# Optimization experiments

Hardware: AMD Instinct MI355X
Metric: run time of the kernel (lower is better)

The kernel has to match this reference:

```python
import jax, jax.numpy as jnp
import numpy as np

V_SRC = 32000; V_TGT = 32000; E = 512; H = 1024; N = 32; LS = 64; LT = 48; PAD = 0


def setup_inputs() -> dict:
    key = jax.random.key(0)
    ks = jax.random.split(key, 12)
    def rn(k, shape, scale):
        return jax.random.normal(k, shape, dtype=jnp.float32) * jnp.float32(scale)
    return {
        "src": jax.random.randint(ks[0], (N, LS), 0, V_SRC, dtype=jnp.int32),
        "tgt": jax.random.randint(ks[1], (N, LT), 0, V_TGT, dtype=jnp.int32),
        "enc_embed": rn(ks[2], (V_SRC, E), 0.02),
        "enc_Wi": rn(ks[3], (E, 4 * H), 1.0 / np.sqrt(E)),
        "enc_Wh": rn(ks[4], (H, 4 * H), 1.0 / np.sqrt(H)),
        "enc_b": jnp.zeros((4 * H,), jnp.float32),
        "dec_embed": rn(ks[5], (V_TGT, E), 0.02),
        "dec_Wi": rn(ks[6], (E + H, 4 * H), 1.0 / np.sqrt(E + H)),
        "dec_Wh": rn(ks[7], (H, 4 * H), 1.0 / np.sqrt(H)),
        "dec_b": jnp.zeros((4 * H,), jnp.float32),
        "attn_W": rn(ks[8], (H, H), 1.0 / np.sqrt(H)),
        "attn_b": jnp.zeros((H,), jnp.float32),
        "h2o_W": rn(ks[9], (H, V_TGT), 1.0 / np.sqrt(H)),
        "h2o_b": jnp.zeros((V_TGT,), jnp.float32),
    }


def _lstm_step(h, c, x, Wi, Wh, b):
    # fused gate GEMM; gate order i, f, g, o (matches the 8 separate Linears)
    gates = x @ Wi + h @ Wh + b
    i, f, g, o = jnp.split(gates, 4, axis=-1)
    c_new = jax.nn.sigmoid(f) * c + jax.nn.sigmoid(i) * jnp.tanh(g)
    h_new = jax.nn.sigmoid(o) * jnp.tanh(c_new)
    return h_new, c_new


def reference(src, tgt, enc_embed, enc_Wi, enc_Wh, enc_b,
              dec_embed, dec_Wi, dec_Wh, dec_b,
              attn_W, attn_b, h2o_W, h2o_b):
    n = src.shape[0]
    h0 = jnp.zeros((n, H), enc_Wi.dtype)
    c0 = jnp.zeros((n, H), enc_Wi.dtype)

    # ---- encoder: scan over source timesteps ----
    emb_src = enc_embed[src]                       # [N,LS,E]
    def estep(carry, x_t):
        h, c = carry
        h, c = _lstm_step(h, c, x_t, enc_Wi, enc_Wh, enc_b)
        return (h, c), h
    (h, c), enc_h = jax.lax.scan(estep, (h0, c0), jnp.swapaxes(emb_src, 0, 1))
    enc_h = jnp.swapaxes(enc_h, 0, 1)              # [N,LS,H]
    mask = (src == PAD)                            # True = PAD

    # Attention linear on encoder_outputs is step-invariant -> precompute once
    energy = enc_h @ attn_W + attn_b               # [N,LS,H]

    # ---- decoder: teacher forcing (ratio=1.0) over tgt[:, :-1] ----
    def dstep(carry, tok):
        h, c = carry
        emb = dec_embed[tok]                       # [N,E]
        scores = jnp.einsum('nlh,nh->nl', energy, h)
        scores = jnp.where(mask, jnp.float32(-1e9), scores)
        w = jax.nn.softmax(scores, axis=1)         # [N,LS]
        ctx = jnp.einsum('nl,nlh->nh', w, enc_h)   # [N,H]
        h, c = _lstm_step(h, c, jnp.concatenate([emb, ctx], axis=-1),
                          dec_Wi, dec_Wh, dec_b)
        out = jax.nn.log_softmax(h @ h2o_W + h2o_b, axis=-1)
        return (h, c), out
    _, outs = jax.lax.scan(dstep, (h, c), jnp.swapaxes(tgt[:, :-1], 0, 1))
    return jnp.swapaxes(outs, 0, 1)                # [N, LT-1, V_TGT]
```

## Files before the change

### kernel.cpp

```cpp
#include <hip/hip_runtime.h>


using u16 = unsigned short;
using u32 = unsigned int;
using bf16x8 = __attribute__((ext_vector_type(8))) __bf16;
using f32x4  = __attribute__((ext_vector_type(4))) float;
using u32x4  = __attribute__((ext_vector_type(4))) unsigned int;
using u32x2  = __attribute__((ext_vector_type(2))) unsigned int;

__device__ __forceinline__ u16 f2bf(float x) {
  u32 u = __float_as_uint(x);
  u32 r = (u + 0x7FFFu + ((u >> 16) & 1u)) >> 16;
  return (u16)r;
}
__device__ __forceinline__ float bf2f(u16 b) { return __uint_as_float(((u32)b) << 16); }
__device__ __forceinline__ float sigm(float x) { return 1.f / (1.f + expf(-x)); }

__device__ __forceinline__ f32x4 mfma16(u32x4 a, u32x4 b, f32x4 c) {
  return __builtin_amdgcn_mfma_f32_16x16x32_bf16(
      __builtin_bit_cast(bf16x8, a), __builtin_bit_cast(bf16x8, b), c, 0, 0, 0);
}

__global__ __launch_bounds__(256)
void k_transpose_split(const float* __restrict__ W, int K, int N,
                       u16* __restrict__ Thi, u16* __restrict__ Tlo,
                       int ldT, int koff)
{
  __shared__ float tile[32][33];
  const int k0 = blockIdx.y << 5, n0 = blockIdx.x << 5;
  const int tx = threadIdx.x & 31, ty = threadIdx.x >> 5;
  #pragma unroll
  for (int i = ty; i < 32; i += 8)
    tile[i][tx] = W[(size_t)(k0 + i) * N + n0 + tx];
  __syncthreads();
  #pragma unroll
  for (int i = ty; i < 32; i += 8) {
    float v = tile[tx][i];
    u16 hi = f2bf(v);
    size_t di = (size_t)(n0 + i) * ldT + koff + k0 + tx;
    Thi[di] = hi;
    if (Tlo) Tlo[di] = f2bf(v - bf2f(hi));
  }
}

__global__ __launch_bounds__(256)
void k_embed(const float* __restrict__ emb, const int* __restrict__ toks,
             int tokStride, int nRows, u16* __restrict__ A)
{
  int id = blockIdx.x * 256 + threadIdx.x;
  if (id >= nRows * 64) return;
  int r = id >> 6, c8 = (id & 63) << 3;
  int t = r >> 5, n = r & 31;
  int tok = toks[n * tokStride + t];
  const float* s = emb + (size_t)tok * 512 + c8;
  f32x4 x0 = *(const f32x4*)s;
  f32x4 x1 = *(const f32x4*)(s + 4);
  u32x4 w;
  w[0] = (u32)f2bf(x0[0]) | ((u32)f2bf(x0[1]) << 16);
  w[1] = (u32)f2bf(x0[2]) | ((u32)f2bf(x0[3]) << 16);
  w[2] = (u32)f2bf(x1[0]) | ((u32)f2bf(x1[1]) << 16);
  w[3] = (u32)f2bf(x1[2]) | ((u32)f2bf(x1[3]) << 16);
  *(u32x4*)(A + (size_t)r * 512 + c8) = w;
}

template<bool X2, int OUTMAP>
__global__ __launch_bounds__(256)
void gemm_k(const u16* __restrict__ Ah, const u16* __restrict__ Al,
            const u16* __restrict__ Bh, const u16* __restrict__ Bl,
            const float* __restrict__ bias, float* __restrict__ C,
            int M, int N, int K, int Mstore)
{
  const int lane = threadIdx.x & 63, wave = threadIdx.x >> 6;
  const int m0 = blockIdx.y * 128 + (wave >> 1) * 64;
  const int n0 = blockIdx.x * 128 + (wave & 1) * 64;
  const int fr = lane & 15, fq = lane >> 4;
  const f32x4 z = {0.f, 0.f, 0.f, 0.f};
  f32x4 acc[4][4];
  #pragma unroll
  for (int i = 0; i < 4; i++)
    #pragma unroll
    for (int j = 0; j < 4; j++) acc[i][j] = z;

  const size_t a_base = (size_t)(m0 + fr) * K + fq * 8;
  const size_t b_base = (size_t)(n0 + fr) * K + fq * 8;
  for (int k0 = 0; k0 < K; k0 += 32) {
    u32x4 a[4], b[4], a2[4], b2[4];
    #pragma unroll
    for (int i = 0; i < 4; i++) a[i] = *(const u32x4*)(Ah + a_base + (size_t)i * 16 * K + k0);
    #pragma unroll
    for (int j = 0; j < 4; j++) b[j] = *(const u32x4*)(Bh + b_base + (size_t)j * 16 * K + k0);
    if constexpr (X2) {
      #pragma unroll
      for (int i = 0; i < 4; i++) a2[i] = *(const u32x4*)(Al + a_base + (size_t)i * 16 * K + k0);
      #pragma unroll
      for (int j = 0; j < 4; j++) b2[j] = *(const u32x4*)(Bl + b_base + (size_t)j * 16 * K + k0);
    }
    #pragma unroll
    for (int i = 0; i < 4; i++)
      #pragma unroll
      for (int j = 0; j < 4; j++) {
        acc[i][j] = mfma16(a[i], b[j], acc[i][j]);
        if constexpr (X2) {
          acc[i][j] = mfma16(a[i], b2[j], acc[i][j]);
          acc[i][j] = mfma16(a2[i], b[j], acc[i][j]);
        }
      }
  }
  #pragma unroll
  for (int i = 0; i < 4; i++) {
    int row_b = m0 + i * 16 + fq * 4;
    #pragma unroll
    for (int j = 0; j < 4; j++) {
      int col = n0 + j * 16 + fr;
      float bv = bias ? bias[col] : 0.f;
      #pragma unroll
      for (int r = 0; r < 4; r++) {
        int row = row_b + r;
        if (row < Mstore) {
          float v = acc[i][j][r] + bv;
          if (OUTMAP) {
            int nn = row & 31, tt = row >> 5;
            C[(size_t)(nn * 47 + tt) * N + col] = v;
          } else {
            C[(size_t)row * N + col] = v;
          }
        }
      }
    }
  }
}

__global__ __launch_bounds__(256)
void rec_gemm(const u16* __restrict__ Ah, const u16* __restrict__ Al,
              const u16* __restrict__ Bh, const u16* __restrict__ Bl,
              float* __restrict__ partial, int KK, int kchunk)
{
  const int lane = threadIdx.x & 63, wave = threadIdx.x >> 6;
  const int n0 = blockIdx.x * 256 + wave * 64;
  const int fr = lane & 15, fq = lane >> 4;
  const int ks = blockIdx.y * kchunk, ke = ks + kchunk;
  const f32x4 z = {0.f, 0.f, 0.f, 0.f};
  f32x4 acc[2][4];
  #pragma unroll
  for (int i = 0; i < 2; i++)
    #pragma unroll
    for (int j = 0; j < 4; j++) acc[i][j] = z;

  for (int k0 = ks; k0 < ke; k0 += 32) {
    u32x4 a[2], a2[2], b[4], b2[4];
    #pragma unroll
    for (int i = 0; i < 2; i++) {
      size_t o = (size_t)(i * 16 + fr) * KK + k0 + fq * 8;
      a[i]  = *(const u32x4*)(Ah + o);
      a2[i] = *(const u32x4*)(Al + o);
    }
    #pragma unroll
    for (int j = 0; j < 4; j++) {
      size_t o = (size_t)(n0 + j * 16 + fr) * KK + k0 + fq * 8;
      b[j]  = *(const u32x4*)(Bh + o);
      b2[j] = *(const u32x4*)(Bl + o);
    }
    #pragma unroll
    for (int i = 0; i < 2; i++)
      #pragma unroll
      for (int j = 0; j < 4; j++) {
        acc[i][j] = mfma16(a[i], b[j], acc[i][j]);
        acc[i][j] = mfma16(a[i], b2[j], acc[i][j]);
        acc[i][j] = mfma16(a2[i], b[j], acc[i][j]);
      }
  }
  float* pb = partial + (size_t)blockIdx.y * 32 * 4096;
  #pragma unroll
  for (int i = 0; i < 2; i++)
    #pragma unroll
    for (int j = 0; j < 4; j++)
      #pragma unroll
      for (int r = 0; r < 4; r++) {
        int row = i * 16 + fq * 4 + r;
        int col = n0 + j * 16 + fr;
        pb[(size_t)row * 4096 + col] = acc[i][j][r];
      }
}

__global__ __launch_bounds__(256)
void point_enc(const float* __restrict__ partial, const float* __restrict__ Xi,
               float* __restrict__ c, float* __restrict__ hf,
               u16* __restrict__ hhi, u16* __restrict__ hlo, int usep)
{
  int idx = blockIdx.x * 256 + threadIdx.x;
  int n = idx >> 10, hh = idx & 1023;
  size_t xb = (size_t)n * 4096 + hh;
  float g[4];
  #pragma unroll
  for (int j = 0; j < 4; j++) {
    float v = Xi[xb + j * 1024];
    if (usep) {
      #pragma unroll
      for (int s = 0; s < 8; s++) v += partial[(size_t)(s * 32 + n) * 4096 + j * 1024 + hh];
    }
    g[j] = v;
  }
  float cp = usep ? c[idx] : 0.f;
  float cn = sigm(g[1]) * cp + sigm(g[0]) * tanhf(g[2]);
  float hv = sigm(g[3]) * tanhf(cn);
  c[idx] = cn;
  hf[idx] = hv;
  u16 hi = f2bf(hv);
  hhi[idx] = hi;
  hlo[idx] = f2bf(hv - bf2f(hi));
}

__global__ __launch_bounds__(256)
void point_dec(const float* __restrict__ partial, const float* __restrict__ Xi,
               float* __restrict__ c, float* __restrict__ hf,
               u16* __restrict__ xh, u16* __restrict__ xl,
               u16* __restrict__ dh, u16* __restrict__ dl)
{
  int idx = blockIdx.x * 256 + threadIdx.x;
  int n = idx >> 10, hh = idx & 1023;
  size_t xb = (size_t)n * 4096 + hh;
  float g[4];
  #pragma unroll
  for (int j = 0; j < 4; j++) {
    float v = Xi[xb + j * 1024];
    #pragma unroll
    for (int s = 0; s < 8; s++) v += partial[(size_t)(s * 32 + n) * 4096 + j * 1024 + hh];
    g[j] = v;
  }
  float cn = sigm(g[1]) * c[idx] + sigm(g[0]) * tanhf(g[2]);
  float hv = sigm(g[3]) * tanhf(cn);
  c[idx] = cn;
  hf[idx] = hv;
  u16 hi = f2bf(hv);
  u16 lo = f2bf(hv - bf2f(hi));
  size_t xo = (size_t)n * 2048 + 1024 + hh;
  xh[xo] = hi; xl[xo] = lo;
  dh[idx] = hi; dl[idx] = lo;
}

__global__ __launch_bounds__(256)
void attn_k(const float* __restrict__ energy, const float* __restrict__ ench,
            const float* __restrict__ h, const int* __restrict__ src,
            u16* __restrict__ xh, u16* __restrict__ xl)
{
  __shared__ float shh[1024];
  __shared__ float red[256];
  __shared__ float sw[64];
  const int n = blockIdx.x, tid = threadIdx.x;
  ((f32x4*)shh)[tid] = ((const f32x4*)(h + ((size_t)n << 10)))[tid];
  __syncthreads();
  {
    int l = tid >> 2, q = tid & 3;
    const float* er = energy + (((size_t)(l * 32 + n)) << 10) + q * 256;
    const float* hc = shh + q * 256;
    float p = 0.f;
    #pragma unroll 8
    for (int j = 0; j < 256; j += 4) {
      f32x4 e4 = *(const f32x4*)(er + j);
      p += e4[0] * hc[j] + e4[1] * hc[j + 1] + e4[2] * hc[j + 2] + e4[3] * hc[j + 3];
    }
    red[tid] = p;
  }
  __syncthreads();
  if (tid < 64) {
    float sco = red[tid * 4] + red[tid * 4 + 1] + red[tid * 4 + 2] + red[tid * 4 + 3];
    if (src[n * 64 + tid] == 0) sco = -1e9f;
    float mm = sco;
    #pragma unroll
    for (int off = 32; off; off >>= 1) mm = fmaxf(mm, __shfl_xor(mm, off));
    float e = __expf(sco - mm), su = e;
    #pragma unroll
    for (int off = 32; off; off >>= 1) su += __shfl_xor(su, off);
    sw[tid] = e / su;
  }
  __syncthreads();
  int c0 = tid * 4;
  float a0 = 0.f, a1 = 0.f, a2 = 0.f, a3 = 0.f;
  for (int l = 0; l < 64; l++) {
    float wl = sw[l];
    const f32x4 v = *(const f32x4*)(ench + (((size_t)(l * 32 + n)) << 10) + c0);
    a0 += wl * v[0]; a1 += wl * v[1]; a2 += wl * v[2]; a3 += wl * v[3];
  }
  u16 h0 = f2bf(a0), h1 = f2bf(a1), h2 = f2bf(a2), h3 = f2bf(a3);
  u16 l0 = f2bf(a0 - bf2f(h0)), l1 = f2bf(a1 - bf2f(h1));
  u16 l2 = f2bf(a2 - bf2f(h2)), l3 = f2bf(a3 - bf2f(h3));
  u32x2 hv, lv;
  hv[0] = (u32)h0 | ((u32)h1 << 16); hv[1] = (u32)h2 | ((u32)h3 << 16);
  lv[0] = (u32)l0 | ((u32)l1 << 16); lv[1] = (u32)l2 | ((u32)l3 << 16);
  *(u32x2*)(xh + (size_t)n * 2048 + c0) = hv;
  *(u32x2*)(xl + (size_t)n * 2048 + c0) = lv;
}

__global__ __launch_bounds__(256)
void k_prep_xcat(const u16* __restrict__ sh, const u16* __restrict__ sl,
                 u16* __restrict__ xh, u16* __restrict__ xl)
{
  int idx = blockIdx.x * 256 + threadIdx.x;
  int n = idx >> 10, hh = idx & 1023;
  size_t xo = (size_t)n * 2048 + 1024 + hh;
  xh[xo] = sh[idx];
  xl[xo] = sl[idx];
}

__global__ __launch_bounds__(256)
void k_logsoftmax(float* __restrict__ out)
{
  float* row = out + (size_t)blockIdx.x * 32000;
  const int tid = threadIdx.x;
  float m = -3.0e38f, s = 0.f;
  for (int i = tid; i < 8000; i += 256) {
    f32x4 x = ((const f32x4*)row)[i];
    #pragma unroll
    for (int j = 0; j < 4; j++) {
      float v = x[j];
      if (v > m) { s = s * __expf(m - v) + 1.f; m = v; }
      else s += __expf(v - m);
    }
  }
  #pragma unroll
  for (int off = 32; off; off >>= 1) {
    float m2 = __shfl_xor(m, off), s2 = __shfl_xor(s, off);
    float M = fmaxf(m, m2);
    s = s * __expf(m - M) + s2 * __expf(m2 - M);
    m = M;
  }
  __shared__ float sm[4], ss[4];
  if ((tid & 63) == 0) { sm[tid >> 6] = m; ss[tid >> 6] = s; }
  __syncthreads();
  float M = fmaxf(fmaxf(sm[0], sm[1]), fmaxf(sm[2], sm[3]));
  float S = ss[0] * __expf(sm[0] - M) + ss[1] * __expf(sm[1] - M) +
            ss[2] * __expf(sm[2] - M) + ss[3] * __expf(sm[3] - M);
  float lse = M + __logf(S);
  for (int i = tid; i < 8000; i += 256) {
    f32x4 x = ((f32x4*)row)[i];
    x[0] -= lse; x[1] -= lse; x[2] -= lse; x[3] -= lse;
    ((f32x4*)row)[i] = x;
  }
}

extern "C" void kernel_launch(void* const* d_in, const int* in_sizes, int n_in,
                              void* d_out, int out_size, void* d_ws, size_t ws_size,
                              hipStream_t stream)
{
  (void)in_sizes; (void)n_in; (void)out_size; (void)ws_size;
  const int*   src  = (const int*)d_in[0];
  const int*   tgt  = (const int*)d_in[1];
  const float* eemb = (const float*)d_in[2];
  const float* eWi  = (const float*)d_in[3];
  const float* eWh  = (const float*)d_in[4];
  const float* eb   = (const float*)d_in[5];
  const float* demb = (const float*)d_in[6];
  const float* dWi  = (const float*)d_in[7];
  const float* dWh  = (const float*)d_in[8];
  const float* db   = (const float*)d_in[9];
  const float* aW   = (const float*)d_in[10];
  const float* ab   = (const float*)d_in[11];
  const float* hW   = (const float*)d_in[12];
  const float* hb   = (const float*)d_in[13];
  float* out = (float*)d_out;

  char* wsp = (char*)d_ws;
  size_t off = 0;
  auto alloc = [&](size_t bytes) -> void* {
    void* p = wsp + off;
    off += (bytes + 255) & ~(size_t)255;
    return p;
  };
  u16* WiTe  = (u16*)alloc((size_t)4096 * 512 * 2);
  u16* WhTh  = (u16*)alloc((size_t)4096 * 1024 * 2);
  u16* WhTl  = (u16*)alloc((size_t)4096 * 1024 * 2);
  u16* DWiTe = (u16*)alloc((size_t)4096 * 512 * 2);
  u16* WcTh  = (u16*)alloc((size_t)4096 * 2048 * 2);
  u16* WcTl  = (u16*)alloc((size_t)4096 * 2048 * 2);
  u16* AwTh  = (u16*)alloc((size_t)1024 * 1024 * 2);
  u16* AwTl  = (u16*)alloc((size_t)1024 * 1024 * 2);
  u16* HoTh  = (u16*)alloc((size_t)32000 * 1024 * 2);
  u16* HoTl  = (u16*)alloc((size_t)32000 * 1024 * 2);
  u16*   Aenc   = (u16*)alloc((size_t)2048 * 512 * 2);
  u16*   Adec   = (u16*)alloc((size_t)1536 * 512 * 2);
  float* XiE    = (float*)alloc((size_t)2048 * 4096 * 4);
  float* XiD    = (float*)alloc((size_t)1536 * 4096 * 4);
  float* ench   = (float*)alloc((size_t)64 * 32 * 1024 * 4);
  u16*   encHh  = (u16*)alloc((size_t)64 * 32 * 1024 * 2);
  u16*   encHl  = (u16*)alloc((size_t)64 * 32 * 1024 * 2);
  float* energy = (float*)alloc((size_t)64 * 32 * 1024 * 4);
  float* cbuf   = (float*)alloc((size_t)32 * 1024 * 4);
  float* hdec   = (float*)alloc((size_t)32 * 1024 * 4);
  u16*   xh     = (u16*)alloc((size_t)32 * 2048 * 2);
  u16*   xl     = (u16*)alloc((size_t)32 * 2048 * 2);
  u16*   dechh  = (u16*)alloc((size_t)1536 * 1024 * 2);
  u16*   dechl  = (u16*)alloc((size_t)1536 * 1024 * 2);
  float* partial = (float*)alloc((size_t)8 * 32 * 4096 * 4);

  dim3 B(256);

  k_transpose_split<<<dim3(128, 16), B, 0, stream>>>(eWi, 512, 4096, WiTe, nullptr, 512, 0);
  k_transpose_split<<<dim3(128, 32), B, 0, stream>>>(eWh, 1024, 4096, WhTh, WhTl, 1024, 0);
  k_transpose_split<<<dim3(128, 16), B, 0, stream>>>(dWi, 512, 4096, DWiTe, nullptr, 512, 0);
  k_transpose_split<<<dim3(128, 32), B, 0, stream>>>(dWi + (size_t)512 * 4096, 1024, 4096, WcTh, WcTl, 2048, 0);
  k_transpose_split<<<dim3(128, 32), B, 0, stream>>>(dWh, 1024, 4096, WcTh, WcTl, 2048, 1024);
  k_transpose_split<<<dim3(32, 32),  B, 0, stream>>>(aW, 1024, 1024, AwTh, AwTl, 1024, 0);
  k_transpose_split<<<dim3(1000, 32), B, 0, stream>>>(hW, 1024, 32000, HoTh, HoTl, 1024, 0);

  k_embed<<<512, B, 0, stream>>>(eemb, src, 64, 2048, Aenc);
  k_embed<<<376, B, 0, stream>>>(demb, tgt, 48, 1504, Adec);

  gemm_k<false, 0><<<dim3(32, 16), B, 0, stream>>>(Aenc, nullptr, WiTe, nullptr, eb, XiE, 2048, 4096, 512, 2048);
  gemm_k<false, 0><<<dim3(32, 12), B, 0, stream>>>(Adec, nullptr, DWiTe, nullptr, db, XiD, 1536, 4096, 512, 1536);

  for (int t = 0; t < 64; t++) {
    if (t > 0)
      rec_gemm<<<dim3(16, 8), B, 0, stream>>>(encHh + (size_t)(t - 1) * 32768,
                                              encHl + (size_t)(t - 1) * 32768,
                                              WhTh, WhTl, partial, 1024, 128);
    point_enc<<<128, B, 0, stream>>>(partial, XiE + (size_t)t * 131072, cbuf,
                                     ench + (size_t)t * 32768,
                                     encHh + (size_t)t * 32768,
                                     encHl + (size_t)t * 32768, t > 0 ? 1 : 0);
  }

  gemm_k<true, 0><<<dim3(8, 16), B, 0, stream>>>(encHh, encHl, AwTh, AwTl, ab, energy, 2048, 1024, 1024, 2048);

  k_prep_xcat<<<128, B, 0, stream>>>(encHh + (size_t)63 * 32768, encHl + (size_t)63 * 32768, xh, xl);
  for (int t = 0; t < 47; t++) {
    const float* hp = (t == 0) ? (ench + (size_t)63 * 32768) : hdec;
    attn_k<<<32, B, 0, stream>>>(energy, ench, hp, src, xh, xl);
    rec_gemm<<<dim3(16, 8), B, 0, stream>>>(xh, xl, WcTh, WcTl, partial, 2048, 256);
    point_dec<<<128, B, 0, stream>>>(partial, XiD + (size_t)t * 131072, cbuf, hdec,
                                     xh, xl,
                                     dechh + (size_t)t * 32768,
                                     dechl + (size_t)t * 32768);
  }

  gemm_k<true, 1><<<dim3(250, 12), B, 0, stream>>>(dechh, dechl, HoTh, HoTl, hb, out, 1536, 32000, 1024, 1504);

  k_logsoftmax<<<1504, B, 0, stream>>>(out);
}
```

Before: 3.827 ms.

## Fuse recurrent GEMM with LSTM pointwise per step; add prefetching h2o GEMM

Replaces the split-K recurrent GEMM plus separate pointwise kernel with one kernel per timestep. Each block computes all four gate columns for 16 hidden units across the full K range, then applies the LSTM cell in shared memory. This removes the partial-sum buffer round trip and one launch per step, but leaves only 64 blocks per step with a long serial K loop. The decoder input buffer is double-buffered so the fused kernel can write the next step's h while still reading the current one. The output projection gets its own 512-thread kernel with 256-row tiles and register prefetch of the next K slice.

```diff
diff --git a/kernel.cpp b/kernel.cpp
--- a/kernel.cpp
+++ b/kernel.cpp
@@ -63,7 +63,7 @@
   *(u32x4*)(A + (size_t)r * 512 + c8) = w;
 }
 
-template<bool X2, int OUTMAP>
+template<bool X2>
 __global__ __launch_bounds__(256)
 void gemm_k(const u16* __restrict__ Ah, const u16* __restrict__ Al,
             const u16* __restrict__ Bh, const u16* __restrict__ Bl,
@@ -116,126 +116,189 @@
       #pragma unroll
       for (int r = 0; r < 4; r++) {
         int row = row_b + r;
-        if (row < Mstore) {
-          float v = acc[i][j][r] + bv;
-          if (OUTMAP) {
-            int nn = row & 31, tt = row >> 5;
-            C[(size_t)(nn * 47 + tt) * N + col] = v;
-          } else {
-            C[(size_t)row * N + col] = v;
-          }
-        }
+        if (row < Mstore) C[(size_t)row * N + col] = acc[i][j][r] + bv;
       }
     }
   }
 }
 
-__global__ __launch_bounds__(256)
-void rec_gemm(const u16* __restrict__ Ah, const u16* __restrict__ Al,
+__global__ __launch_bounds__(512)
+void gemm_h2o(const u16* __restrict__ Ah, const u16* __restrict__ Al,
               const u16* __restrict__ Bh, const u16* __restrict__ Bl,
-              float* __restrict__ partial, int KK, int kchunk)
+              const float* __restrict__ bias, float* __restrict__ C)
 {
   const int lane = threadIdx.x & 63, wave = threadIdx.x >> 6;
-  const int n0 = blockIdx.x * 256 + wave * 64;
+  const int m0 = blockIdx.y * 256 + (wave >> 1) * 64;
+  const int n0 = blockIdx.x * 128 + (wave & 1) * 64;
   const int fr = lane & 15, fq = lane >> 4;
-  const int ks = blockIdx.y * kchunk, ke = ks + kchunk;
   const f32x4 z = {0.f, 0.f, 0.f, 0.f};
-  f32x4 acc[2][4];
-  #pragma unroll
-  for (int i = 0; i < 2; i++)
+  f32x4 acc[4][4];
+  #pragma unroll
+  for (int i = 0; i < 4; i++)
     #pragma unroll
     for (int j = 0; j < 4; j++) acc[i][j] = z;
 
-  for (int k0 = ks; k0 < ke; k0 += 32) {
-    u32x4 a[2], a2[2], b[4], b2[4];
-    #pragma unroll
-    for (int i = 0; i < 2; i++) {
-      size_t o = (size_t)(i * 16 + fr) * KK + k0 + fq * 8;
-      a[i]  = *(const u32x4*)(Ah + o);
-      a2[i] = *(const u32x4*)(Al + o);
-    }
-    #pragma unroll
-    for (int j = 0; j < 4; j++) {
-      size_t o = (size_t)(n0 + j * 16 + fr) * KK + k0 + fq * 8;
-      b[j]  = *(const u32x4*)(Bh + o);
-      b2[j] = *(const u32x4*)(Bl + o);
-    }
-    #pragma unroll
-    for (int i = 0; i < 2; i++)
+  const size_t ab = (size_t)(m0 + fr) * 1024 + fq * 8;
+  const size_t bb = (size_t)(n0 + fr) * 1024 + fq * 8;
+  u32x4 a[4], a2[4], b[4], b2[4], na[4], na2[4], nb[4], nb2[4];
+  #pragma unroll
+  for (int i = 0; i < 4; i++) {
+    a[i]  = *(const u32x4*)(Ah + ab + (size_t)i * 16 * 1024);
+    a2[i] = *(const u32x4*)(Al + ab + (size_t)i * 16 * 1024);
+    b[i]  = *(const u32x4*)(Bh + bb + (size_t)i * 16 * 1024);
+    b2[i] = *(const u32x4*)(Bl + bb + (size_t)i * 16 * 1024);
+  }
+  for (int k0 = 0; k0 < 1024; k0 += 32) {
+    const bool pf = (k0 + 32) < 1024;
+    if (pf) {
+      #pragma unroll
+      for (int i = 0; i < 4; i++) {
+        na[i]  = *(const u32x4*)(Ah + ab + (size_t)i * 16 * 1024 + k0 + 32);
+        na2[i] = *(const u32x4*)(Al + ab + (size_t)i * 16 * 1024 + k0 + 32);
+        nb[i]  = *(const u32x4*)(Bh + bb + (size_t)i * 16 * 1024 + k0 + 32);
+        nb2[i] = *(const u32x4*)(Bl + bb + (size_t)i * 16 * 1024 + k0 + 32);
+      }
+    }
+    #pragma unroll
+    for (int i = 0; i < 4; i++)
       #pragma unroll
       for (int j = 0; j < 4; j++) {
         acc[i][j] = mfma16(a[i], b[j], acc[i][j]);
         acc[i][j] = mfma16(a[i], b2[j], acc[i][j]);
         acc[i][j] = mfma16(a2[i], b[j], acc[i][j]);
       }
-  }
-  float* pb = partial + (size_t)blockIdx.y * 32 * 4096;
-  #pragma unroll
-  for (int i = 0; i < 2; i++)
-    #pragma unroll
-    for (int j = 0; j < 4; j++)
+    if (pf) {
+      #pragma unroll
+      for (int i = 0; i < 4; i++) { a[i]=na[i]; a2[i]=na2[i]; b[i]=nb[i]; b2[i]=nb2[i]; }
+    }
+  }
+  #pragma unroll
+  for (int i = 0; i < 4; i++) {
+    int row_b = m0 + i * 16 + fq * 4;
+    #pragma unroll
+    for (int j = 0; j < 4; j++) {
+      int col = n0 + j * 16 + fr;
+      float bv = bias[col];
       #pragma unroll
       for (int r = 0; r < 4; r++) {
-        int row = i * 16 + fq * 4 + r;
-        int col = n0 + j * 16 + fr;
-        pb[(size_t)row * 4096 + col] = acc[i][j][r];
+        int row = row_b + r;
+        if (row < 1504) {
+          int nn = row & 31, tt = row >> 5;
+          C[(size_t)(nn * 47 + tt) * 32000 + col] = acc[i][j][r] + bv;
+        }
       }
-}
-
-__global__ __launch_bounds__(256)
-void point_enc(const float* __restrict__ partial, const float* __restrict__ Xi,
-               float* __restrict__ c, float* __restrict__ hf,
-               u16* __restrict__ hhi, u16* __restrict__ hlo, int usep)
-{
-  int idx = blockIdx.x * 256 + threadIdx.x;
-  int n = idx >> 10, hh = idx & 1023;
-  size_t xb = (size_t)n * 4096 + hh;
-  float g[4];
-  #pragma unroll
-  for (int j = 0; j < 4; j++) {
-    float v = Xi[xb + j * 1024];
-    if (usep) {
-      #pragma unroll
-      for (int s = 0; s < 8; s++) v += partial[(size_t)(s * 32 + n) * 4096 + j * 1024 + hh];
-    }
-    g[j] = v;
-  }
-  float cp = usep ? c[idx] : 0.f;
-  float cn = sigm(g[1]) * cp + sigm(g[0]) * tanhf(g[2]);
-  float hv = sigm(g[3]) * tanhf(cn);
-  c[idx] = cn;
-  hf[idx] = hv;
-  u16 hi = f2bf(hv);
-  hhi[idx] = hi;
-  hlo[idx] = f2bf(hv - bf2f(hi));
-}
-
-__global__ __launch_bounds__(256)
-void point_dec(const float* __restrict__ partial, const float* __restrict__ Xi,
-               float* __restrict__ c, float* __restrict__ hf,
-               u16* __restrict__ xh, u16* __restrict__ xl,
-               u16* __restrict__ dh, u16* __restrict__ dl)
-{
-  int idx = blockIdx.x * 256 + threadIdx.x;
-  int n = idx >> 10, hh = idx & 1023;
-  size_t xb = (size_t)n * 4096 + hh;
-  float g[4];
-  #pragma unroll
-  for (int j = 0; j < 4; j++) {
-    float v = Xi[xb + j * 1024];
-    #pragma unroll
-    for (int s = 0; s < 8; s++) v += partial[(size_t)(s * 32 + n) * 4096 + j * 1024 + hh];
-    g[j] = v;
-  }
-  float cn = sigm(g[1]) * c[idx] + sigm(g[0]) * tanhf(g[2]);
-  float hv = sigm(g[3]) * tanhf(cn);
-  c[idx] = cn;
-  hf[idx] = hv;
-  u16 hi = f2bf(hv);
-  u16 lo = f2bf(hv - bf2f(hi));
-  size_t xo = (size_t)n * 2048 + 1024 + hh;
-  xh[xo] = hi; xl[xo] = lo;
-  dh[idx] = hi; dl[idx] = lo;
+    }
+  }
+}
+
+__global__ __launch_bounds__(256)
+void enc_step(const u16* __restrict__ hh, const u16* __restrict__ hl,
+              const u16* __restrict__ Bh, const u16* __restrict__ Bl,
+              const float* __restrict__ Xi, float* __restrict__ c,
+              float* __restrict__ hf,
+              u16* __restrict__ ohh, u16* __restrict__ ohl, int first)
+{
+  const int lane = threadIdx.x & 63, wave = threadIdx.x >> 6;
+  const int fr = lane & 15, fq = lane >> 4;
+  const int s0 = blockIdx.x << 4;
+  __shared__ float g4[4][32][16];
+  f32x4 acc0 = {0.f, 0.f, 0.f, 0.f}, acc1 = acc0;
+  if (!first) {
+    const size_t bbase = (size_t)(wave * 1024 + s0 + fr) * 1024 + fq * 8;
+    const size_t abase = (size_t)fr * 1024 + fq * 8;
+    for (int k0 = 0; k0 < 1024; k0 += 32) {
+      u32x4 b   = *(const u32x4*)(Bh + bbase + k0);
+      u32x4 b2  = *(const u32x4*)(Bl + bbase + k0);
+      u32x4 a0  = *(const u32x4*)(hh + abase + k0);
+      u32x4 a0l = *(const u32x4*)(hl + abase + k0);
+      u32x4 a1  = *(const u32x4*)(hh + abase + 16 * 1024 + k0);
+      u32x4 a1l = *(const u32x4*)(hl + abase + 16 * 1024 + k0);
+      acc0 = mfma16(a0, b, acc0); acc0 = mfma16(a0, b2, acc0); acc0 = mfma16(a0l, b, acc0);
+      acc1 = mfma16(a1, b, acc1); acc1 = mfma16(a1, b2, acc1); acc1 = mfma16(a1l, b, acc1);
+    }
+  }
+  #pragma unroll
+  for (int r = 0; r < 4; r++) {
+    g4[wave][fq * 4 + r][fr] = acc0[r];
+    g4[wave][16 + fq * 4 + r][fr] = acc1[r];
+  }
+  __syncthreads();
+  #pragma unroll
+  for (int e = 0; e < 2; e++) {
+    int idx = threadIdx.x * 2 + e;
+    int n = idx >> 4, cc = idx & 15;
+    int hcol = s0 + cc;
+    size_t gx = (size_t)n * 4096 + hcol;
+    float gi = Xi[gx] + g4[0][n][cc];
+    float gf = Xi[gx + 1024] + g4[1][n][cc];
+    float gg = Xi[gx + 2048] + g4[2][n][cc];
+    float go = Xi[gx + 3072] + g4[3][n][cc];
+    size_t ho = (size_t)n * 1024 + hcol;
+    float cp = first ? 0.f : c[ho];
+    float cn = sigm(gf) * cp + sigm(gi) * tanhf(gg);
+    float hv = sigm(go) * tanhf(cn);
+    c[ho] = cn;
+    hf[ho] = hv;
+    u16 hi = f2bf(hv);
+    ohh[ho] = hi;
+    ohl[ho] = f2bf(hv - bf2f(hi));
+  }
+}
+
+__global__ __launch_bounds__(256)
+void dec_step(const u16* __restrict__ xinh, const u16* __restrict__ xinl,
+              const u16* __restrict__ Bh, const u16* __restrict__ Bl,
+              const float* __restrict__ Xi, float* __restrict__ c,
+              float* __restrict__ hf,
+              u16* __restrict__ xouth, u16* __restrict__ xoutl,
+              u16* __restrict__ dh, u16* __restrict__ dl)
+{
+  const int lane = threadIdx.x & 63, wave = threadIdx.x >> 6;
+  const int fr = lane & 15, fq = lane >> 4;
+  const int s0 = blockIdx.x << 4;
+  __shared__ float g4[4][32][16];
+  f32x4 acc0 = {0.f, 0.f, 0.f, 0.f}, acc1 = acc0;
+  {
+    const size_t bbase = (size_t)(wave * 1024 + s0 + fr) * 2048 + fq * 8;
+    const size_t abase = (size_t)fr * 2048 + fq * 8;
+    for (int k0 = 0; k0 < 2048; k0 += 32) {
+      u32x4 b   = *(const u32x4*)(Bh + bbase + k0);
+      u32x4 b2  = *(const u32x4*)(Bl + bbase + k0);
+      u32x4 a0  = *(const u32x4*)(xinh + abase + k0);
+      u32x4 a0l = *(const u32x4*)(xinl + abase + k0);
+      u32x4 a1  = *(const u32x4*)(xinh + abase + 16 * 2048 + k0);
+      u32x4 a1l = *(const u32x4*)(xinl + abase + 16 * 2048 + k0);
+      acc0 = mfma16(a0, b, acc0); acc0 = mfma16(a0, b2, acc0); acc0 = mfma16(a0l, b, acc0);
+      acc1 = mfma16(a1, b, acc1); acc1 = mfma16(a1, b2, acc1); acc1 = mfma16(a1l, b, acc1);
+    }
+  }
+  #pragma unroll
+  for (int r = 0; r < 4; r++) {
+    g4[wave][fq * 4 + r][fr] = acc0[r];
+    g4[wave][16 + fq * 4 + r][fr] = acc1[r];
+  }
+  __syncthreads();
+  #pragma unroll
+  for (int e = 0; e < 2; e++) {
+    int idx = threadIdx.x * 2 + e;
+    int n = idx >> 4, cc = idx & 15;
+    int hcol = s0 + cc;
+    size_t gx = (size_t)n * 4096 + hcol;
+    float gi = Xi[gx] + g4[0][n][cc];
+    float gf = Xi[gx + 1024] + g4[1][n][cc];
+    float gg = Xi[gx + 2048] + g4[2][n][cc];
+    float go = Xi[gx + 3072] + g4[3][n][cc];
+    size_t ho = (size_t)n * 1024 + hcol;
+    float cn = sigm(gf) * c[ho] + sigm(gi) * tanhf(gg);
+    float hv = sigm(go) * tanhf(cn);
+    c[ho] = cn;
+    hf[ho] = hv;
+    u16 hi = f2bf(hv);
+    u16 lo = f2bf(hv - bf2f(hi));
+    size_t xo = (size_t)n * 2048 + 1024 + hcol;
+    xouth[xo] = hi; xoutl[xo] = lo;
+    dh[ho] = hi; dl[ho] = lo;
+  }
 }
 
 __global__ __launch_bounds__(256)
@@ -386,11 +449,12 @@
   float* energy = (float*)alloc((size_t)64 * 32 * 1024 * 4);
   float* cbuf   = (float*)alloc((size_t)32 * 1024 * 4);
   float* hdec   = (float*)alloc((size_t)32 * 1024 * 4);
-  u16*   xh     = (u16*)alloc((size_t)32 * 2048 * 2);
-  u16*   xl     = (u16*)alloc((size_t)32 * 2048 * 2);
+  u16*   xh0    = (u16*)alloc((size_t)32 * 2048 * 2);
+  u16*   xl0    = (u16*)alloc((size_t)32 * 2048 * 2);
+  u16*   xh1    = (u16*)alloc((size_t)32 * 2048 * 2);
+  u16*   xl1    = (u16*)alloc((size_t)32 * 2048 * 2);
   u16*   dechh  = (u16*)alloc((size_t)1536 * 1024 * 2);
   u16*   dechl  = (u16*)alloc((size_t)1536 * 1024 * 2);
-  float* partial = (float*)alloc((size_t)8 * 32 * 4096 * 4);
 
   dim3 B(256);
 
@@ -405,34 +469,35 @@
   k_embed<<<512, B, 0, stream>>>(eemb, src, 64, 2048, Aenc);
   k_embed<<<376, B, 0, stream>>>(demb, tgt, 48, 1504, Adec);
 
-  gemm_k<false, 0><<<dim3(32, 16), B, 0, stream>>>(Aenc, nullptr, WiTe, nullptr, eb, XiE, 2048, 4096, 512, 2048);
-  gemm_k<false, 0><<<dim3(32, 12), B, 0, stream>>>(Adec, nullptr, DWiTe, nullptr, db, XiD, 1536, 4096, 512, 1536);
+  gemm_k<false><<<dim3(32, 16), B, 0, stream>>>(Aenc, nullptr, WiTe, nullptr, eb, XiE, 2048, 4096, 512, 2048);
+  gemm_k<false><<<dim3(32, 12), B, 0, stream>>>(Adec, nullptr, DWiTe, nullptr, db, XiD, 1536, 4096, 512, 1536);
 
   for (int t = 0; t < 64; t++) {
-    if (t > 0)
-      rec_gemm<<<dim3(16, 8), B, 0, stream>>>(encHh + (size_t)(t - 1) * 32768,
-                                              encHl + (size_t)(t - 1) * 32768,
-                                              WhTh, WhTl, partial, 1024, 128);
-    point_enc<<<128, B, 0, stream>>>(partial, XiE + (size_t)t * 131072, cbuf,
-                                     ench + (size_t)t * 32768,
-                                     encHh + (size_t)t * 32768,
-                                     encHl + (size_t)t * 32768, t > 0 ? 1 : 0);
-  }
-
-  gemm_k<true, 0><<<dim3(8, 16), B, 0, stream>>>(encHh, encHl, AwTh, AwTl, ab, energy, 2048, 1024, 1024, 2048);
-
-  k_prep_xcat<<<128, B, 0, stream>>>(encHh + (size_t)63 * 32768, encHl + (size_t)63 * 32768, xh, xl);
+    const u16* ph = encHh + (size_t)(t > 0 ? t - 1 : 0) * 32768;
+    const u16* pl = encHl + (size_t)(t > 0 ? t - 1 : 0) * 32768;
+    enc_step<<<64, B, 0, stream>>>(ph, pl, WhTh, WhTl,
+                                   XiE + (size_t)t * 131072, cbuf,
+                                   ench + (size_t)t * 32768,
+                                   encHh + (size_t)t * 32768,
+                                   encHl + (size_t)t * 32768, t == 0 ? 1 : 0);
+  }
+
+  gemm_k<true><<<dim3(8, 16), B, 0, stream>>>(encHh, encHl, AwTh, AwTl, ab, energy, 2048, 1024, 1024, 2048);
+
+  k_prep_xcat<<<128, B, 0, stream>>>(encHh + (size_t)63 * 32768, encHl + (size_t)63 * 32768, xh0, xl0);
   for (int t = 0; t < 47; t++) {
+    u16* xinh = (t & 1) ? xh1 : xh0; u16* xinl = (t & 1) ? xl1 : xl0;
+    u16* xouh = (t & 1) ? xh0 : xh1; u16* xoul = (t & 1) ? xl0 : xl1;
     const float* hp = (t == 0) ? (ench + (size_t)63 * 32768) : hdec;
-    attn_k<<<32, B, 0, stream>>>(energy, ench, hp, src, xh, xl);
-    rec_gemm<<<dim3(16, 8), B, 0, stream>>>(xh, xl, WcTh, WcTl, partial, 2048, 256);
-    point_dec<<<128, B, 0, stream>>>(partial, XiD + (size_t)t * 131072, cbuf, hdec,
-                                     xh, xl,
-                                     dechh + (size_t)t * 32768,
-                                     dechl + (size_t)t * 32768);
-  }
-
-  gemm_k<true, 1><<<dim3(250, 12), B, 0, stream>>>(dechh, dechl, HoTh, HoTl, hb, out, 1536, 32000, 1024, 1504);
+    attn_k<<<32, B, 0, stream>>>(energy, ench, hp, src, xinh, xinl);
+    dec_step<<<64, B, 0, stream>>>(xinh, xinl, WcTh, WcTl,
+                                   XiD + (size_t)t * 131072, cbuf, hdec,
+                                   xouh, xoul,
+                                   dechh + (size_t)t * 32768,
+                                   dechl + (size_t)t * 32768);
+  }
+
+  gemm_h2o<<<dim3(250, 6), dim3(512), 0, stream>>>(dechh, dechl, HoTh, HoTl, hb, out);
 
   k_logsoftmax<<<1504, B, 0, stream>>>(out);
 }
```

New measurement: 6.000 ms. 1.57x slower.
